# Kernel optimization log

Measured on AMD Instinct MI355X. Metric: run time of the kernel, lower is better.

## Reference

```python
import jax, jax.numpy as jnp
import numpy as np

N_LEVELS = 16
N_FEAT = 2
LOG2_T = 19
T = 2 ** LOG2_T
BASE_RES = 2 ** 4
MAX_RES = 2 ** 11
PER_LEVEL_SCALE = np.exp((np.log(MAX_RES) - np.log(BASE_RES)) / (N_LEVELS - 1))
RESOLUTIONS = [int(np.floor(BASE_RES * PER_LEVEL_SCALE ** lv)) + 1 for lv in range(N_LEVELS)]
INIT_ACTIVE_LEVEL = 8
N_POINTS = 1048576
N_OUT = N_LEVELS * N_FEAT
# tcnn spatial hashing primes
P1 = jnp.uint32(2654435761)
P2 = jnp.uint32(805459861)


def _level_lookup(x, tbl, res):
    """x: [N,3] in [0,1], tbl: [T,F], res: python int grid resolution."""
    pos = x * (res - 1)                       # [N,3]
    c0 = jnp.clip(jnp.floor(pos).astype(jnp.int32), 0, res - 2)
    w = pos - c0.astype(pos.dtype)            # [N,3] trilinear fractions
    feats = jnp.zeros((x.shape[0], tbl.shape[-1]), dtype=tbl.dtype)
    dense = (res ** 3) <= T                   # static per level: dense grid vs hashed
    for dz in (0, 1):
        for dy in (0, 1):
            for dx in (0, 1):
                offs = jnp.array([dx, dy, dz], jnp.int32)
                c = c0 + offs                 # [N,3] corner int coords
                if dense:
                    idx = c[:, 0] + res * (c[:, 1] + res * c[:, 2])
                else:
                    cu = c.astype(jnp.uint32)
                    idx = ((cu[:, 0]) ^ (cu[:, 1] * P1) ^ (cu[:, 2] * P2)) & jnp.uint32(T - 1)
                    idx = idx.astype(jnp.int32)
                # trilinear corner weight: prod over axes of (w if offs==1 else 1-w)
                wc = jnp.prod(jnp.where(offs == 1, w, 1.0 - w), axis=-1)  # [N]
                feats = feats + tbl[idx] * wc[:, None]
    return feats


def setup_inputs() -> dict:
    key = jax.random.key(0)
    k1, k2 = jax.random.split(key)
    x = jax.random.uniform(k1, (N_POINTS, 3), dtype=jnp.float32)
    # tcnn-style small uniform init of the hash table
    table = jax.random.uniform(k2, (N_LEVELS, T, N_FEAT), dtype=jnp.float32,
                               minval=-1e-4, maxval=1e-4)
    mask = jnp.concatenate([
        jnp.ones(INIT_ACTIVE_LEVEL * N_FEAT, jnp.float32),
        jnp.zeros((N_LEVELS - INIT_ACTIVE_LEVEL) * N_FEAT, jnp.float32),
    ])
    return {"x": x, "table": table, "mask": mask}


def reference(x, table, mask):
    # multi-resolution hash grid encoding + progressive level mask
    outs = [_level_lookup(x, table[lv], RESOLUTIONS[lv]) for lv in range(N_LEVELS)]
    enc = jnp.concatenate(outs, axis=-1)      # [N, 32]
    return enc * mask
```

## Files before the change

kernel.cpp:

```cpp
#include <hip/hip_runtime.h>
#include <cstdint>
#include <cstddef>


namespace {

constexpr int      kNLevels = 16;
constexpr uint32_t kT       = 1u << 19;
constexpr uint32_t kP1      = 2654435761u;
constexpr uint32_t kP2      = 805459861u;

typedef float v2f __attribute__((ext_vector_type(2)));
typedef float v4f __attribute__((ext_vector_type(4)));

__device__ constexpr int kRes[kNLevels] = {
    17, 23, 31, 43, 59, 81, 112, 154, 213, 295, 407, 562, 777, 1073, 1483, 2049
};

__device__ inline void corner_setup(float px, float py, float pz, int res,
                                    int& cx, int& cy, int& cz,
                                    float& wx, float& wy, float& wz) {
    const float s = (float)(res - 1);
    const float fx = px * s, fy = py * s, fz = pz * s;
    cx = (int)floorf(fx); cy = (int)floorf(fy); cz = (int)floorf(fz);
    cx = min(max(cx, 0), res - 2);
    cy = min(max(cy, 0), res - 2);
    cz = min(max(cz, 0), res - 2);
    wx = fx - (float)cx; wy = fy - (float)cy; wz = fz - (float)cz;
}

__global__ __launch_bounds__(256) void hashed_level_kernel(
    const float* __restrict__ x, const float* __restrict__ table,
    const float* __restrict__ mask, float* __restrict__ ws, int n)
{
    const int lv = 5 + blockIdx.y;
    const float m0 = mask[2 * lv], m1 = mask[2 * lv + 1];
    if (m0 == 0.0f && m1 == 0.0f) return;

    const int p = blockIdx.x * blockDim.x + threadIdx.x;
    if (p >= n) return;
    const float px = x[3 * p + 0];
    const float py = x[3 * p + 1];
    const float pz = x[3 * p + 2];

    const int res = kRes[lv];
    int cx, cy, cz; float wx, wy, wz;
    corner_setup(px, py, pz, res, cx, cy, cz, wx, wy, wz);
    const float ux = 1.0f - wx, uy = 1.0f - wy, uz = 1.0f - wz;
    const float* __restrict__ tbl = table + (size_t)lv * (size_t)(kT * 2);

    float r0 = 0.0f, r1 = 0.0f;
#pragma unroll
    for (int c = 0; c < 8; ++c) {
        const int dx = c & 1, dy = (c >> 1) & 1, dz = (c >> 2) & 1;
        const uint32_t idx =
            (((uint32_t)(cx + dx)) ^ ((uint32_t)(cy + dy) * kP1)
                                   ^ ((uint32_t)(cz + dz) * kP2)) & (kT - 1u);
        const v2f v = *(const v2f*)(tbl + 2u * idx);
        const float w = (dx ? wx : ux) * (dy ? wy : uy) * (dz ? wz : uz);
        r0 = fmaf(v.x, w, r0);
        r1 = fmaf(v.y, w, r1);
    }
    v2f o; o.x = r0; o.y = r1;
    __builtin_nontemporal_store(
        o, (v2f*)(ws + ((size_t)(lv - 5) * n + p) * 2));
}

__global__ __launch_bounds__(256) void gather_out_kernel(
    const float* __restrict__ x, const float* __restrict__ table,
    const float* __restrict__ ws, const float* __restrict__ mask,
    float* __restrict__ out, int n)
{
    const int p = blockIdx.x * blockDim.x + threadIdx.x;
    if (p >= n) return;
    const float px = x[3 * p + 0];
    const float py = x[3 * p + 1];
    const float pz = x[3 * p + 2];

    v4f o[8];

#pragma unroll
    for (int lv = 0; lv < 5; ++lv) {
        const float m0 = mask[2 * lv], m1 = mask[2 * lv + 1];
        float r0 = 0.0f, r1 = 0.0f;
        if (m0 != 0.0f || m1 != 0.0f) {
            const int res = kRes[lv];
            int cx, cy, cz; float wx, wy, wz;
            corner_setup(px, py, pz, res, cx, cy, cz, wx, wy, wz);
            const float ux = 1.0f - wx, uy = 1.0f - wy, uz = 1.0f - wz;
            const float* __restrict__ tbl = table + (size_t)lv * (size_t)(kT * 2);
#pragma unroll
            for (int c = 0; c < 4; ++c) {
                const int dy = c & 1, dz = (c >> 1) & 1;
                const uint32_t idx0 =
                    (uint32_t)(cx + res * ((cy + dy) + res * (cz + dz)));
                v4f ab;
                __builtin_memcpy(&ab, tbl + 2u * idx0, sizeof(v4f));
                const float wyz = (dy ? wy : uy) * (dz ? wz : uz);
                const float w0 = ux * wyz, w1 = wx * wyz;
                r0 = fmaf(ab.x, w0, fmaf(ab.z, w1, r0));
                r1 = fmaf(ab.y, w0, fmaf(ab.w, w1, r1));
            }
            r0 *= m0; r1 *= m1;
        }
        if (lv & 1) { o[lv >> 1].z = r0; o[lv >> 1].w = r1; }
        else        { o[lv >> 1].x = r0; o[lv >> 1].y = r1; }
    }

#pragma unroll
    for (int lv = 5; lv < kNLevels; ++lv) {
        const float m0 = mask[2 * lv], m1 = mask[2 * lv + 1];
        float r0 = 0.0f, r1 = 0.0f;
        if (m0 != 0.0f || m1 != 0.0f) {
            const v2f v = __builtin_nontemporal_load(
                (const v2f*)(ws + ((size_t)(lv - 5) * n + p) * 2));
            r0 = v.x * m0;
            r1 = v.y * m1;
        }
        if (lv & 1) { o[lv >> 1].z = r0; o[lv >> 1].w = r1; }
        else        { o[lv >> 1].x = r0; o[lv >> 1].y = r1; }
    }

    v4f* __restrict__ op = (v4f*)(out + (size_t)p * 32);
#pragma unroll
    for (int i = 0; i < 8; ++i) op[i] = o[i];
}

__global__ __launch_bounds__(256) void fused_kernel(
    const float* __restrict__ x, const float* __restrict__ table,
    const float* __restrict__ mask, float* __restrict__ out, int n)
{
    const int p = blockIdx.x * blockDim.x + threadIdx.x;
    if (p >= n) return;
    const float px = x[3 * p + 0], py = x[3 * p + 1], pz = x[3 * p + 2];
    v4f o[8];
#pragma unroll
    for (int lv = 0; lv < kNLevels; ++lv) {
        const float m0 = mask[2 * lv], m1 = mask[2 * lv + 1];
        float r0 = 0.0f, r1 = 0.0f;
        if (m0 != 0.0f || m1 != 0.0f) {
            const int res = kRes[lv];
            const bool dense = ((long long)res * res * res) <= (long long)kT;
            int cx, cy, cz; float wx, wy, wz;
            corner_setup(px, py, pz, res, cx, cy, cz, wx, wy, wz);
            const float ux = 1.0f - wx, uy = 1.0f - wy, uz = 1.0f - wz;
            const float* __restrict__ tbl = table + (size_t)lv * (size_t)(kT * 2);
#pragma unroll
            for (int c = 0; c < 8; ++c) {
                const int dx = c & 1, dy = (c >> 1) & 1, dz = (c >> 2) & 1;
                const int ix = cx + dx, iy = cy + dy, iz = cz + dz;
                uint32_t idx;
                if (dense) idx = (uint32_t)(ix + res * (iy + res * iz));
                else idx = (((uint32_t)ix) ^ ((uint32_t)iy * kP1)
                                           ^ ((uint32_t)iz * kP2)) & (kT - 1u);
                const v2f v = *(const v2f*)(tbl + 2u * idx);
                const float w = (dx ? wx : ux) * (dy ? wy : uy) * (dz ? wz : uz);
                r0 = fmaf(v.x, w, r0);
                r1 = fmaf(v.y, w, r1);
            }
            r0 *= m0; r1 *= m1;
        }
        if (lv & 1) { o[lv >> 1].z = r0; o[lv >> 1].w = r1; }
        else        { o[lv >> 1].x = r0; o[lv >> 1].y = r1; }
    }
    v4f* __restrict__ op = (v4f*)(out + (size_t)p * 32);
#pragma unroll
    for (int i = 0; i < 8; ++i) op[i] = o[i];
}

}

extern "C" void kernel_launch(void* const* d_in, const int* in_sizes, int n_in,
                              void* d_out, int out_size, void* d_ws, size_t ws_size,
                              hipStream_t stream) {
    const float* x     = (const float*)d_in[0];
    const float* table = (const float*)d_in[1];
    const float* mask  = (const float*)d_in[2];
    float*       out   = (float*)d_out;

    const int n = in_sizes[0] / 3;
    const int block = 256;
    const int gx = (n + block - 1) / block;

    const size_t ws_needed = (size_t)(kNLevels - 5) * (size_t)n * 2 * sizeof(float);
    if (ws_size >= ws_needed) {
        float* ws = (float*)d_ws;
        dim3 grid1(gx, kNLevels - 5);
        hashed_level_kernel<<<grid1, block, 0, stream>>>(x, table, mask, ws, n);
        gather_out_kernel<<<gx, block, 0, stream>>>(x, table, ws, mask, out, n);
    } else {
        fused_kernel<<<gx, block, 0, stream>>>(x, table, mask, out, n);
    }
}
```

Measured before the change: 350.9 us.

## Pair adjacent hashed corners into vec4 loads and stage output through LDS

```diff
diff --git a/kernel.cpp b/kernel.cpp
--- a/kernel.cpp
+++ b/kernel.cpp
@@ -49,17 +49,35 @@
     const float ux = 1.0f - wx, uy = 1.0f - wy, uz = 1.0f - wz;
     const float* __restrict__ tbl = table + (size_t)lv * (size_t)(kT * 2);
 
+    const uint32_t hy0 = (uint32_t)cy * kP1, hy1 = (uint32_t)(cy + 1) * kP1;
+    const uint32_t hz0 = (uint32_t)cz * kP2, hz1 = (uint32_t)(cz + 1) * kP2;
+    const uint32_t cxu = (uint32_t)cx;
+
     float r0 = 0.0f, r1 = 0.0f;
-#pragma unroll
-    for (int c = 0; c < 8; ++c) {
-        const int dx = c & 1, dy = (c >> 1) & 1, dz = (c >> 2) & 1;
-        const uint32_t idx =
-            (((uint32_t)(cx + dx)) ^ ((uint32_t)(cy + dy) * kP1)
-                                   ^ ((uint32_t)(cz + dz) * kP2)) & (kT - 1u);
-        const v2f v = *(const v2f*)(tbl + 2u * idx);
-        const float w = (dx ? wx : ux) * (dy ? wy : uy) * (dz ? wz : uz);
-        r0 = fmaf(v.x, w, r0);
-        r1 = fmaf(v.y, w, r1);
+    if ((cx & 1) == 0) {
+#pragma unroll
+        for (int c = 0; c < 4; ++c) {
+            const uint32_t h = ((c & 1) ? hy1 : hy0) ^ ((c >> 1) ? hz1 : hz0);
+            const uint32_t i0 = (cxu ^ h) & (kT - 1u);
+            const v4f ab = *(const v4f*)(tbl + 2u * (i0 & ~1u));
+            const float wyz = ((c & 1) ? wy : uy) * ((c >> 1) ? wz : uz);
+            const float w0 = ux * wyz, w1 = wx * wyz;
+            const bool sw = (i0 & 1u) != 0u;
+            r0 = fmaf(sw ? ab.z : ab.x, w0, fmaf(sw ? ab.x : ab.z, w1, r0));
+            r1 = fmaf(sw ? ab.w : ab.y, w0, fmaf(sw ? ab.y : ab.w, w1, r1));
+        }
+    } else {
+#pragma unroll
+        for (int c = 0; c < 8; ++c) {
+            const int dx = c & 1, dy = (c >> 1) & 1, dz = (c >> 2) & 1;
+            const uint32_t idx =
+                ((cxu + (uint32_t)dx) ^ (dy ? hy1 : hy0) ^ (dz ? hz1 : hz0))
+                & (kT - 1u);
+            const v2f v = *(const v2f*)(tbl + 2u * idx);
+            const float w = (dx ? wx : ux) * (dy ? wy : uy) * (dz ? wz : uz);
+            r0 = fmaf(v.x, w, r0);
+            r1 = fmaf(v.y, w, r1);
+        }
     }
     v2f o; o.x = r0; o.y = r1;
     __builtin_nontemporal_store(
@@ -71,11 +89,15 @@
     const float* __restrict__ ws, const float* __restrict__ mask,
     float* __restrict__ out, int n)
 {
-    const int p = blockIdx.x * blockDim.x + threadIdx.x;
-    if (p >= n) return;
-    const float px = x[3 * p + 0];
-    const float py = x[3 * p + 1];
-    const float pz = x[3 * p + 2];
+    __shared__ float lds[128 * 32];
+
+    const int tid = threadIdx.x;
+    const int p   = blockIdx.x * 256 + tid;
+    const int pc  = (p < n) ? p : (n - 1);
+
+    const float px = x[3 * pc + 0];
+    const float py = x[3 * pc + 1];
+    const float pz = x[3 * pc + 2];
 
     v4f o[8];
 
@@ -113,7 +135,7 @@
         float r0 = 0.0f, r1 = 0.0f;
         if (m0 != 0.0f || m1 != 0.0f) {
             const v2f v = __builtin_nontemporal_load(
-                (const v2f*)(ws + ((size_t)(lv - 5) * n + p) * 2));
+                (const v2f*)(ws + ((size_t)(lv - 5) * n + pc) * 2));
             r0 = v.x * m0;
             r1 = v.y * m1;
         }
@@ -121,9 +143,29 @@
         else        { o[lv >> 1].x = r0; o[lv >> 1].y = r1; }
     }
 
-    v4f* __restrict__ op = (v4f*)(out + (size_t)p * 32);
-#pragma unroll
-    for (int i = 0; i < 8; ++i) op[i] = o[i];
+    const int r    = tid & 127;
+    const int half = tid >> 7;
+#pragma unroll
+    for (int h = 0; h < 2; ++h) {
+        if (h) __syncthreads();
+        if (half == h) {
+#pragma unroll
+            for (int c = 0; c < 8; ++c)
+                *(v4f*)&lds[r * 32 + ((c ^ (r & 7)) << 2)] = o[c];
+        }
+        __syncthreads();
+        const long long bp = (long long)blockIdx.x * 256 + h * 128;
+        float* const obase = out + (size_t)bp * 32;
+#pragma unroll
+        for (int j = 0; j < 4; ++j) {
+            const int m  = tid + 256 * j;
+            const int pr = m >> 3, c = m & 7;
+            if (bp + pr < n) {
+                const v4f v = *(const v4f*)&lds[pr * 32 + ((c ^ (pr & 7)) << 2)];
+                __builtin_nontemporal_store(v, (v4f*)obase + m);
+            }
+        }
+    }
 }
 
 __global__ __launch_bounds__(256) void fused_kernel(
```

New measurement: 326.0 us. 7.1% less time.
